# Kernel tuning notes

Measured on AMD Instinct MI355X. Metric: run time of the kernel, lower is better.

The kernel has to match this reference:

```python
import jax, jax.numpy as jnp
import numpy as np

D_MODEL = 2048
N_HEADS = 16
N_KV_HEADS = 4
D_K = D_MODEL // N_HEADS  # 128
N_REP = N_HEADS // N_KV_HEADS  # 4
EPS = 1e-8
ROPE_BASE = 10000.0


def setup_inputs() -> dict:
    key = jax.random.key(0)
    ks = jax.random.split(key, 6)
    B, S = 2, 2048
    s_in = 1.0 / np.sqrt(D_MODEL)
    return {
        "x": jax.random.normal(ks[0], (B, S, D_MODEL), jnp.float32),
        "Wq": jax.random.normal(ks[1], (D_MODEL, D_MODEL), jnp.float32) * s_in,
        "bq": jnp.zeros((D_MODEL,), jnp.float32),
        "Wk": jax.random.normal(ks[2], (N_KV_HEADS * D_K, D_MODEL), jnp.float32) * s_in,
        "bk": jnp.zeros((N_KV_HEADS * D_K,), jnp.float32),
        "Wv": jax.random.normal(ks[3], (N_KV_HEADS * D_K, D_MODEL), jnp.float32) * s_in,
        "bv": jnp.zeros((N_KV_HEADS * D_K,), jnp.float32),
        "Wo": jax.random.normal(ks[4], (D_MODEL, D_MODEL), jnp.float32) * s_in,
        "bo": jnp.zeros((D_MODEL,), jnp.float32),
        "q_norm_w": jnp.ones((D_K,), jnp.float32),
        "k_norm_w": jnp.ones((D_K,), jnp.float32),
    }


def _rmsnorm(x, w):
    rms = jnp.sqrt(jnp.mean(x * x, axis=-1, keepdims=True) + EPS)
    return x / rms * w


def _rope(x, cos, sin):
    # x: [B, S, H, d_k]; interleaved pair rotation (pairs along last dim)
    B, S, H, d = x.shape
    xr = x.reshape(B, S, H, d // 2, 2)
    x1, x2 = xr[..., 0], xr[..., 1]
    c = cos[:, None, :]  # [S, 1, d/2] -> broadcasts over [B, S, H, d/2]
    s = sin[:, None, :]
    o1 = x1 * c - x2 * s
    o2 = x1 * s + x2 * c
    return jnp.stack([o1, o2], axis=-1).reshape(B, S, H, d)


def reference(x, Wq, bq, Wk, bk, Wv, bv, Wo, bo, q_norm_w, k_norm_w):
    B, S, D = x.shape
    scale = 1.0 / np.sqrt(D_K)

    q = (x @ Wq.T + bq).reshape(B, S, N_HEADS, D_K)
    k = (x @ Wk.T + bk).reshape(B, S, N_KV_HEADS, D_K)
    v = (x @ Wv.T + bv).reshape(B, S, N_KV_HEADS, D_K)

    q = _rmsnorm(q, q_norm_w)
    k = _rmsnorm(k, k_norm_w)

    # RoPE tables (cos/sin of t * inv_freq), shape [S, d_k/2]
    inv_freq = 1.0 / (ROPE_BASE ** (jnp.arange(0, D_K, 2, dtype=jnp.float32) / D_K))
    freqs = jnp.arange(S, dtype=jnp.float32)[:, None] * inv_freq[None, :]
    cos, sin = jnp.cos(freqs), jnp.sin(freqs)
    q = _rope(q, cos, sin)
    k = _rope(k, cos, sin)

    # [B, H, S, d]
    q = q.transpose(0, 2, 1, 3)
    k = k.transpose(0, 2, 1, 3)
    v = v.transpose(0, 2, 1, 3)

    # GQA: group q heads by kv head instead of repeating k/v
    qg = q.reshape(B, N_KV_HEADS, N_REP, S, D_K)
    scores = jnp.einsum("bkrqd,bkld->bkrql", qg, k) * scale
    causal = jnp.tril(jnp.ones((S, S), dtype=bool))  # [S, S]
    scores = jnp.where(causal, scores, jnp.float32(-1e9))
    attn = jax.nn.softmax(scores, axis=-1)
    out = jnp.einsum("bkrql,bkld->bkrqd", attn, v)  # [B, Hk, rep, S, d]
    out = out.reshape(B, N_HEADS, S, D_K).transpose(0, 2, 1, 3).reshape(B, S, D)
    return out @ Wo.T + bo
```

## Files before the change

kernel.cpp:

```cpp
#include <hip/hip_runtime.h>
#include <hip/hip_bf16.h>
#include <stdint.h>

#define DM 2048
#define SQ 2048
#define NB 2
#define NH 16
#define NKV 4
#define DK 128
#define NQKV 3072

typedef unsigned short u16;
typedef unsigned int u32;
typedef __attribute__((ext_vector_type(8))) __bf16 bf16x8;
typedef __attribute__((ext_vector_type(4))) float f32x4;
typedef __attribute__((ext_vector_type(8))) u16 u16x8;
typedef __attribute__((ext_vector_type(2))) u32 u32x2;

__device__ __forceinline__ u16 f2bf(float f) {
  u32 x = __builtin_bit_cast(u32, f);
  x += 0x7fffu + ((x >> 16) & 1u);
  return (u16)(x >> 16);
}

__device__ __forceinline__ f32x4 mfma16(bf16x8 a, bf16x8 b, f32x4 c) {
  return __builtin_amdgcn_mfma_f32_16x16x32_bf16(a, b, c, 0, 0, 0);
}

#define GLDS16(g, l)                                                          \
  __builtin_amdgcn_global_load_lds(                                           \
      (const __attribute__((address_space(1))) void*)(g),                     \
      (__attribute__((address_space(3))) void*)(l), 16, 0, 0)

__global__ void cast_kernel(const float* __restrict__ src, u16* __restrict__ dst, int n8) {
  int i = blockIdx.x * blockDim.x + threadIdx.x;
  if (i >= n8) return;
  const float4* s4 = (const float4*)src;
  float4 a = s4[2 * i], b = s4[2 * i + 1];
  u16x8 v;
  v[0] = f2bf(a.x); v[1] = f2bf(a.y); v[2] = f2bf(a.z); v[3] = f2bf(a.w);
  v[4] = f2bf(b.x); v[5] = f2bf(b.y); v[6] = f2bf(b.z); v[7] = f2bf(b.w);
  *(u16x8*)(dst + 8 * (size_t)i) = v;
}

__global__ void fuse_bias(const float* __restrict__ bq, const float* __restrict__ bk,
                          const float* __restrict__ bv, float* __restrict__ fb) {
  int i = blockIdx.x * blockDim.x + threadIdx.x;
  if (i >= NQKV) return;
  float v;
  if (i < DM) v = bq[i];
  else if (i < DM + NKV * DK) v = bk[i - DM];
  else v = bv[i - DM - NKV * DK];
  fb[i] = v;
}

__global__ __launch_bounds__(256) void gemm_bt(
    const u16* __restrict__ A, const u16* __restrict__ W,
    const float* __restrict__ bias, float* __restrict__ C,
    int M, int N, int K) {
  __shared__ u16 As[128 * 64];
  __shared__ u16 Bs[128 * 64];
  const int tid = threadIdx.x;
  const int w = tid >> 6, l = tid & 63;
  const int hi = l >> 4, lo = l & 15;
  const int MB = M >> 7;
  const int nwg = gridDim.x;
  const int bid = blockIdx.x;
  const int swz = (bid & 7) * (nwg >> 3) + (bid >> 3);
  const int bm = swz % MB, bn = swz / MB;
  const int wr = w >> 1, wc = w & 1;
  const int lr8 = l >> 3, lc = l & 7;
  f32x4 acc[4][4] = {};
  for (int kt = 0; kt < K; kt += 64) {
#pragma unroll
    for (int i = 0; i < 4; ++i) {
      int row = w * 32 + i * 8 + lr8;
      int gc = lc ^ (row & 7);
      GLDS16(A + (size_t)(bm * 128 + row) * K + kt + gc * 8, &As[(w * 32 + i * 8) * 64]);
    }
#pragma unroll
    for (int i = 0; i < 4; ++i) {
      int row = w * 32 + i * 8 + lr8;
      int gc = lc ^ (row & 7);
      GLDS16(W + (size_t)(bn * 128 + row) * K + kt + gc * 8, &Bs[(w * 32 + i * 8) * 64]);
    }
    __syncthreads();
#pragma unroll
    for (int kk = 0; kk < 2; ++kk) {
      bf16x8 af[4], bf[4];
#pragma unroll
      for (int mi = 0; mi < 4; ++mi) {
        int row = wr * 64 + mi * 16 + lo;
        af[mi] = *(const bf16x8*)&As[row * 64 + (((kk * 4 + hi) ^ (row & 7)) * 8)];
      }
#pragma unroll
      for (int ni = 0; ni < 4; ++ni) {
        int row = wc * 64 + ni * 16 + lo;
        bf[ni] = *(const bf16x8*)&Bs[row * 64 + (((kk * 4 + hi) ^ (row & 7)) * 8)];
      }
#pragma unroll
      for (int mi = 0; mi < 4; ++mi)
#pragma unroll
        for (int ni = 0; ni < 4; ++ni)
          acc[mi][ni] = mfma16(af[mi], bf[ni], acc[mi][ni]);
    }
    __syncthreads();
  }
#pragma unroll
  for (int mi = 0; mi < 4; ++mi) {
#pragma unroll
    for (int ni = 0; ni < 4; ++ni) {
      int col = bn * 128 + wc * 64 + ni * 16 + lo;
      float bv = bias[col];
#pragma unroll
      for (int r = 0; r < 4; ++r) {
        int rowg = bm * 128 + wr * 64 + mi * 16 + hi * 4 + r;
        C[(size_t)rowg * N + col] = acc[mi][ni][r] + bv;
      }
    }
  }
}

__global__ void normrope_qk(const float* __restrict__ qkv,
                            const float* __restrict__ qw, const float* __restrict__ kw,
                            u16* __restrict__ qb, u16* __restrict__ kb) {
  int gw = (int)((blockIdx.x * (size_t)blockDim.x + threadIdx.x) >> 6);
  int lane = threadIdx.x & 63;
  int bs = gw / (NH + NKV), j = gw % (NH + NKV);
  int b = bs / SQ, s = bs % SQ;
  const float* src;
  const float* wgt;
  u16* dst;
  float post = 1.0f;
  if (j < NH) {
    src = qkv + (size_t)bs * NQKV + j * DK;
    wgt = qw;
    dst = qb + ((size_t)(b * NH + j) * SQ + s) * DK;
    post = 0.08838834764831845f;
  } else {
    int kh = j - NH;
    src = qkv + (size_t)bs * NQKV + DM + kh * DK;
    wgt = kw;
    dst = kb + ((size_t)(b * NKV + kh) * SQ + s) * DK;
  }
  float2 xv = *(const float2*)(src + 2 * lane);
  float ss = xv.x * xv.x + xv.y * xv.y;
#pragma unroll
  for (int m = 1; m < 64; m <<= 1) ss += __shfl_xor(ss, m);
  float inv = rsqrtf(ss * (1.0f / DK) + 1e-8f);
  float x1 = xv.x * inv * wgt[2 * lane];
  float x2 = xv.y * inv * wgt[2 * lane + 1];
  float theta = (float)s * expf((float)lane * (-9.2103403720f / 64.0f));
  float sn, cs;
  sincosf(theta, &sn, &cs);
  float o1 = (x1 * cs - x2 * sn) * post;
  float o2 = (x1 * sn + x2 * cs) * post;
  u32 pack = (u32)f2bf(o1) | ((u32)f2bf(o2) << 16);
  *(u32*)(dst + 2 * lane) = pack;
}

__global__ __launch_bounds__(256) void vtrans(const float* __restrict__ qkv, u16* __restrict__ vt) {
  __shared__ u16 T[128 * 72];
  int bid = blockIdx.x;
  int st = bid % (SQ / 64);
  int rem = bid / (SQ / 64);
  int vh = rem % NKV, b = rem / NKV;
  int s0 = st * 64;
  int t = threadIdx.x;
#pragma unroll
  for (int it = 0; it < 8; ++it) {
    int idx = it * 256 + t;
    int sl = idx >> 5;
    int c4 = idx & 31;
    float4 v = *(const float4*)(qkv + (size_t)(b * SQ + s0 + sl) * NQKV + DM + NKV * DK + vh * DK + c4 * 4);
    T[(c4 * 4 + 0) * 72 + sl] = f2bf(v.x);
    T[(c4 * 4 + 1) * 72 + sl] = f2bf(v.y);
    T[(c4 * 4 + 2) * 72 + sl] = f2bf(v.z);
    T[(c4 * 4 + 3) * 72 + sl] = f2bf(v.w);
  }
  __syncthreads();
#pragma unroll
  for (int it = 0; it < 4; ++it) {
    int idx = it * 256 + t;
    int d = idx >> 3;
    int ch = idx & 7;
    u16x8 v = *(const u16x8*)&T[d * 72 + ch * 8];
    *(u16x8*)(vt + ((size_t)(b * NKV + vh) * DK + d) * SQ + s0 + ch * 8) = v;
  }
}

__global__ __launch_bounds__(256) void attn(const u16* __restrict__ qb, const u16* __restrict__ kb,
                                            const u16* __restrict__ vt, u16* __restrict__ out) {
  __shared__ u16 Ks[2][64 * 128];
  __shared__ u16 Vs[2][128 * 64];
  __shared__ u16 P[4][16 * 64];
  const int w = threadIdx.x >> 6, l = threadIdx.x & 63;
  const int hi = l >> 4, lo = l & 15;
  const int pr = blockIdx.x, h = blockIdx.y, b = blockIdx.z;
  const int kvh = h >> 2;
  const u16* Q = qb + (size_t)(b * NH + h) * SQ * DK;
  const u16* K = kb + (size_t)(b * NKV + kvh) * SQ * DK;
  const u16* V = vt + (size_t)(b * NKV + kvh) * DK * SQ;

  auto stageKV = [&](int buf, int kt) {
#pragma unroll
    for (int i = 0; i < 4; ++i) {
      int rb = w * 16 + i * 4;
      int row = rb + (l >> 4);
      int gc = (l & 15) ^ (row & 7);
      GLDS16(K + (size_t)(kt + row) * DK + gc * 8, &Ks[buf][rb * 128]);
    }
#pragma unroll
    for (int i = 0; i < 4; ++i) {
      int rb = w * 32 + i * 8;
      int row = rb + (l >> 3);
      int gc = (l & 7) ^ (row & 7);
      GLDS16(V + (size_t)row * SQ + kt + gc * 8, &Vs[buf][rb * 64]);
    }
  };

#pragma unroll 1
  for (int seg = 0; seg < 2; ++seg) {
    const int qt = seg ? (SQ / 64 - 1 - pr) : pr;
    const int q0 = qt * 64 + w * 16;
    bf16x8 qf[4];
#pragma unroll
    for (int kk = 0; kk < 4; ++kk)
      qf[kk] = *(const bf16x8*)(Q + (size_t)(q0 + lo) * DK + kk * 32 + hi * 8);
    f32x4 oacc[8] = {};
    float lrun = 0.f;
    const int nt = qt + 1;
    stageKV(0, 0);
    __syncthreads();
#pragma unroll 1
    for (int ti = 0; ti < nt; ++ti) {
      const int cur = ti & 1;
      if (ti + 1 < nt) stageKV(cur ^ 1, (ti + 1) * 64);
      const int kt = ti * 64;
      f32x4 sfr[4];
      __builtin_amdgcn_s_setprio(1);
#pragma unroll
      for (int cb = 0; cb < 4; ++cb) {
        f32x4 sf = {};
#pragma unroll
        for (int kk = 0; kk < 4; ++kk) {
          int row = cb * 16 + lo;
          bf16x8 kfr = *(const bf16x8*)&Ks[cur][row * 128 + (((kk * 4 + hi) ^ (row & 7)) * 8)];
          sf = mfma16(kfr, qf[kk], sf);
        }
        sfr[cb] = sf;
      }
      __builtin_amdgcn_s_setprio(0);
      if (ti == nt - 1) {
#pragma unroll
        for (int cb = 0; cb < 4; ++cb)
#pragma unroll
          for (int r = 0; r < 4; ++r) {
            int kcol = kt + cb * 16 + hi * 4 + r;
            if (kcol > q0 + lo) sfr[cb][r] = -1e9f;
          }
      }
      float rs = 0.f;
#pragma unroll
      for (int cb = 0; cb < 4; ++cb) {
        float p0 = __expf(sfr[cb][0] - 12.0f);
        float p1 = __expf(sfr[cb][1] - 12.0f);
        float p2 = __expf(sfr[cb][2] - 12.0f);
        float p3 = __expf(sfr[cb][3] - 12.0f);
        rs += (p0 + p1) + (p2 + p3);
        u32x2 pw;
        pw[0] = (u32)f2bf(p0) | ((u32)f2bf(p1) << 16);
        pw[1] = (u32)f2bf(p2) | ((u32)f2bf(p3) << 16);
        int chunk = cb * 2 + (hi >> 1);
        *(u32x2*)&P[w][lo * 64 + ((chunk ^ (lo & 7)) * 8) + (hi & 1) * 4] = pw;
      }
      rs += __shfl_xor(rs, 16);
      rs += __shfl_xor(rs, 32);
      lrun += rs;
      __builtin_amdgcn_s_setprio(1);
#pragma unroll
      for (int half = 0; half < 2; ++half) {
        bf16x8 pa = *(const bf16x8*)&P[w][lo * 64 + (((half * 4 + hi) ^ (lo & 7)) * 8)];
#pragma unroll
        for (int fr = 0; fr < 8; ++fr) {
          int row = fr * 16 + lo;
          bf16x8 vfr = *(const bf16x8*)&Vs[cur][row * 64 + (((half * 4 + hi) ^ (row & 7)) * 8)];
          oacc[fr] = mfma16(pa, vfr, oacc[fr]);
        }
      }
      __builtin_amdgcn_s_setprio(0);
      __syncthreads();
    }
    float invl = 1.0f / lrun;
    float invlB[4];
#pragma unroll
    for (int r = 0; r < 4; ++r) invlB[r] = __shfl(invl, hi * 4 + r);
#pragma unroll
    for (int fr = 0; fr < 8; ++fr) {
#pragma unroll
      for (int r = 0; r < 4; ++r) {
        int row = b * SQ + q0 + hi * 4 + r;
        int col = h * DK + fr * 16 + lo;
        out[(size_t)row * DM + col] = f2bf(oacc[fr][r] * invlB[r]);
      }
    }
  }
}

extern "C" void kernel_launch(void* const* d_in, const int* in_sizes, int n_in,
                              void* d_out, int out_size, void* d_ws, size_t ws_size,
                              hipStream_t stream) {
  const float* x = (const float*)d_in[0];
  const float* Wq = (const float*)d_in[1];
  const float* bq = (const float*)d_in[2];
  const float* Wk = (const float*)d_in[3];
  const float* bk = (const float*)d_in[4];
  const float* Wv = (const float*)d_in[5];
  const float* bv = (const float*)d_in[6];
  const float* Wo = (const float*)d_in[7];
  const float* bo = (const float*)d_in[8];
  const float* qw = (const float*)d_in[9];
  const float* kw = (const float*)d_in[10];
  float* outp = (float*)d_out;

  char* ws = (char*)d_ws;
  size_t off = 0;
  auto alloc = [&](size_t bytes) {
    char* p = ws + off;
    off += (bytes + 255) & ~(size_t)255;
    return p;
  };
  u16* xb = (u16*)alloc((size_t)NB * SQ * DM * 2);
  u16* Wqkvb = (u16*)alloc((size_t)NQKV * DM * 2);
  u16* Wob = (u16*)alloc((size_t)DM * DM * 2);
  float* fbias = (float*)alloc((size_t)NQKV * 4);
  float* qkvf = (float*)alloc((size_t)NB * SQ * NQKV * 4);
  u16* qbh = (u16*)alloc((size_t)NB * NH * SQ * DK * 2);
  u16* kbh = (u16*)alloc((size_t)NB * NKV * SQ * DK * 2);
  u16* vth = (u16*)alloc((size_t)NB * NKV * DK * SQ * 2);
  u16* aout = (u16*)alloc((size_t)NB * SQ * DM * 2);

  {
    int n8 = NB * SQ * DM / 8;
    cast_kernel<<<(n8 + 255) / 256, 256, 0, stream>>>(x, xb, n8);
    n8 = DM * DM / 8;
    cast_kernel<<<(n8 + 255) / 256, 256, 0, stream>>>(Wq, Wqkvb, n8);
    cast_kernel<<<(n8 + 255) / 256, 256, 0, stream>>>(Wo, Wob, n8);
    n8 = NKV * DK * DM / 8;
    cast_kernel<<<(n8 + 255) / 256, 256, 0, stream>>>(Wk, Wqkvb + (size_t)DM * DM, n8);
    cast_kernel<<<(n8 + 255) / 256, 256, 0, stream>>>(Wv, Wqkvb + (size_t)(DM + NKV * DK) * DM, n8);
    fuse_bias<<<(NQKV + 255) / 256, 256, 0, stream>>>(bq, bk, bv, fbias);
  }
  {
    int M = NB * SQ;
    gemm_bt<<<(M / 128) * (NQKV / 128), 256, 0, stream>>>(xb, Wqkvb, fbias, qkvf, M, NQKV, DM);
  }
  {
    int waves = NB * SQ * (NH + NKV);
    normrope_qk<<<waves / 4, 256, 0, stream>>>(qkvf, qw, kw, qbh, kbh);
    vtrans<<<NB * NKV * (SQ / 64), 256, 0, stream>>>(qkvf, vth);
  }
  {
    dim3 g(SQ / 128, NH, NB);
    attn<<<g, 256, 0, stream>>>(qbh, kbh, vth, aout);
  }
  {
    int M = NB * SQ;
    gemm_bt<<<(M / 128) * (DM / 128), 256, 0, stream>>>(aout, Wob, bo, outp, M, DM, DM);
  }
}
```

Measured before the change: 235.8 us.

## Fuse setup casts, store QKV intermediate in bf16, precompute RoPE tables

```diff
diff --git a/kernel.cpp b/kernel.cpp
--- a/kernel.cpp
+++ b/kernel.cpp
@@ -23,6 +23,11 @@
   return (u16)(x >> 16);
 }
 
+__device__ __forceinline__ float bf2f(u16 h) {
+  u32 x = ((u32)h) << 16;
+  return __builtin_bit_cast(float, x);
+}
+
 __device__ __forceinline__ f32x4 mfma16(bf16x8 a, bf16x8 b, f32x4 c) {
   return __builtin_amdgcn_mfma_f32_16x16x32_bf16(a, b, c, 0, 0, 0);
 }
@@ -32,42 +37,60 @@
       (const __attribute__((address_space(1))) void*)(g),                     \
       (__attribute__((address_space(3))) void*)(l), 16, 0, 0)
 
-__global__ void cast_kernel(const float* __restrict__ src, u16* __restrict__ dst, int n8) {
+#define N_CAST 2359296
+#define N_ROPE (SQ * 64)
+__global__ void setup_all(const float* __restrict__ x, const float* __restrict__ Wq,
+                          const float* __restrict__ Wk, const float* __restrict__ Wv,
+                          const float* __restrict__ Wo, const float* __restrict__ bq,
+                          const float* __restrict__ bk, const float* __restrict__ bv,
+                          u16* __restrict__ xb, u16* __restrict__ Wqkvb, u16* __restrict__ Wob,
+                          float* __restrict__ ct, float* __restrict__ st_,
+                          float* __restrict__ fb) {
   int i = blockIdx.x * blockDim.x + threadIdx.x;
-  if (i >= n8) return;
-  const float4* s4 = (const float4*)src;
-  float4 a = s4[2 * i], b = s4[2 * i + 1];
-  u16x8 v;
-  v[0] = f2bf(a.x); v[1] = f2bf(a.y); v[2] = f2bf(a.z); v[3] = f2bf(a.w);
-  v[4] = f2bf(b.x); v[5] = f2bf(b.y); v[6] = f2bf(b.z); v[7] = f2bf(b.w);
-  *(u16x8*)(dst + 8 * (size_t)i) = v;
-}
-
-__global__ void fuse_bias(const float* __restrict__ bq, const float* __restrict__ bk,
-                          const float* __restrict__ bv, float* __restrict__ fb) {
-  int i = blockIdx.x * blockDim.x + threadIdx.x;
-  if (i >= NQKV) return;
-  float v;
-  if (i < DM) v = bq[i];
-  else if (i < DM + NKV * DK) v = bk[i - DM];
-  else v = bv[i - DM - NKV * DK];
-  fb[i] = v;
+  if (i < N_CAST) {
+    const float* src;
+    u16* dst;
+    int j;
+    if (i < 1048576) { src = x; dst = xb; j = i; }
+    else if (i < 1572864) { src = Wq; dst = Wqkvb; j = i - 1048576; }
+    else if (i < 1703936) { src = Wk; dst = Wqkvb + (size_t)DM * DM; j = i - 1572864; }
+    else if (i < 1835008) { src = Wv; dst = Wqkvb + (size_t)(DM + NKV * DK) * DM; j = i - 1703936; }
+    else { src = Wo; dst = Wob; j = i - 1835008; }
+    const float4* s4 = (const float4*)src;
+    float4 a = s4[2 * j], b = s4[2 * j + 1];
+    u16x8 v;
+    v[0] = f2bf(a.x); v[1] = f2bf(a.y); v[2] = f2bf(a.z); v[3] = f2bf(a.w);
+    v[4] = f2bf(b.x); v[5] = f2bf(b.y); v[6] = f2bf(b.z); v[7] = f2bf(b.w);
+    *(u16x8*)(dst + 8 * (size_t)j) = v;
+  } else if (i < N_CAST + N_ROPE) {
+    int j = i - N_CAST;
+    int s = j >> 6, d = j & 63;
+    float theta = (float)s * __expf((float)d * (-9.2103403720f / 64.0f));
+    float sn, cs;
+    sincosf(theta, &sn, &cs);
+    ct[j] = cs;
+    st_[j] = sn;
+  } else if (i < N_CAST + N_ROPE + NQKV) {
+    int j = i - N_CAST - N_ROPE;
+    float v;
+    if (j < DM) v = bq[j];
+    else if (j < DM + NKV * DK) v = bk[j - DM];
+    else v = bv[j - DM - NKV * DK];
+    fb[j] = v;
+  }
 }
 
 __global__ __launch_bounds__(256) void gemm_bt(
     const u16* __restrict__ A, const u16* __restrict__ W,
-    const float* __restrict__ bias, float* __restrict__ C,
-    int M, int N, int K) {
+    const float* __restrict__ bias, void* __restrict__ Cv,
+    int M, int N, int K, int obf16) {
   __shared__ u16 As[128 * 64];
   __shared__ u16 Bs[128 * 64];
   const int tid = threadIdx.x;
   const int w = tid >> 6, l = tid & 63;
   const int hi = l >> 4, lo = l & 15;
   const int MB = M >> 7;
-  const int nwg = gridDim.x;
-  const int bid = blockIdx.x;
-  const int swz = (bid & 7) * (nwg >> 3) + (bid >> 3);
-  const int bm = swz % MB, bn = swz / MB;
+  const int bm = blockIdx.x % MB, bn = blockIdx.x / MB;
   const int wr = w >> 1, wc = w & 1;
   const int lr8 = l >> 3, lc = l & 7;
   f32x4 acc[4][4] = {};
@@ -115,20 +138,25 @@
 #pragma unroll
       for (int r = 0; r < 4; ++r) {
         int rowg = bm * 128 + wr * 64 + mi * 16 + hi * 4 + r;
-        C[(size_t)rowg * N + col] = acc[mi][ni][r] + bv;
-      }
-    }
-  }
-}
-
-__global__ void normrope_qk(const float* __restrict__ qkv,
+        float val = acc[mi][ni][r] + bv;
+        if (obf16)
+          ((u16*)Cv)[(size_t)rowg * N + col] = f2bf(val);
+        else
+          ((float*)Cv)[(size_t)rowg * N + col] = val;
+      }
+    }
+  }
+}
+
+__global__ void normrope_qk(const u16* __restrict__ qkv,
                             const float* __restrict__ qw, const float* __restrict__ kw,
+                            const float* __restrict__ cosT, const float* __restrict__ sinT,
                             u16* __restrict__ qb, u16* __restrict__ kb) {
   int gw = (int)((blockIdx.x * (size_t)blockDim.x + threadIdx.x) >> 6);
   int lane = threadIdx.x & 63;
   int bs = gw / (NH + NKV), j = gw % (NH + NKV);
   int b = bs / SQ, s = bs % SQ;
-  const float* src;
+  const u16* src;
   const float* wgt;
   u16* dst;
   float post = 1.0f;
@@ -143,23 +171,24 @@
     wgt = kw;
     dst = kb + ((size_t)(b * NKV + kh) * SQ + s) * DK;
   }
-  float2 xv = *(const float2*)(src + 2 * lane);
-  float ss = xv.x * xv.x + xv.y * xv.y;
+  u32 pk = *(const u32*)(src + 2 * lane);
+  float xv0 = bf2f((u16)(pk & 0xffff));
+  float xv1 = bf2f((u16)(pk >> 16));
+  float ss = xv0 * xv0 + xv1 * xv1;
 #pragma unroll
   for (int m = 1; m < 64; m <<= 1) ss += __shfl_xor(ss, m);
   float inv = rsqrtf(ss * (1.0f / DK) + 1e-8f);
-  float x1 = xv.x * inv * wgt[2 * lane];
-  float x2 = xv.y * inv * wgt[2 * lane + 1];
-  float theta = (float)s * expf((float)lane * (-9.2103403720f / 64.0f));
-  float sn, cs;
-  sincosf(theta, &sn, &cs);
+  float x1 = xv0 * inv * wgt[2 * lane];
+  float x2 = xv1 * inv * wgt[2 * lane + 1];
+  float cs = cosT[s * 64 + lane];
+  float sn = sinT[s * 64 + lane];
   float o1 = (x1 * cs - x2 * sn) * post;
   float o2 = (x1 * sn + x2 * cs) * post;
   u32 pack = (u32)f2bf(o1) | ((u32)f2bf(o2) << 16);
   *(u32*)(dst + 2 * lane) = pack;
 }
 
-__global__ __launch_bounds__(256) void vtrans(const float* __restrict__ qkv, u16* __restrict__ vt) {
+__global__ __launch_bounds__(256) void vtrans(const u16* __restrict__ qkv, u16* __restrict__ vt) {
   __shared__ u16 T[128 * 72];
   int bid = blockIdx.x;
   int st = bid % (SQ / 64);
@@ -168,15 +197,13 @@
   int s0 = st * 64;
   int t = threadIdx.x;
 #pragma unroll
-  for (int it = 0; it < 8; ++it) {
+  for (int it = 0; it < 4; ++it) {
     int idx = it * 256 + t;
-    int sl = idx >> 5;
-    int c4 = idx & 31;
-    float4 v = *(const float4*)(qkv + (size_t)(b * SQ + s0 + sl) * NQKV + DM + NKV * DK + vh * DK + c4 * 4);
-    T[(c4 * 4 + 0) * 72 + sl] = f2bf(v.x);
-    T[(c4 * 4 + 1) * 72 + sl] = f2bf(v.y);
-    T[(c4 * 4 + 2) * 72 + sl] = f2bf(v.z);
-    T[(c4 * 4 + 3) * 72 + sl] = f2bf(v.w);
+    int sl = idx >> 4;
+    int c = idx & 15;
+    u16x8 v = *(const u16x8*)(qkv + (size_t)(b * SQ + s0 + sl) * NQKV + DM + NKV * DK + vh * DK + c * 8);
+#pragma unroll
+    for (int e = 0; e < 8; ++e) T[(c * 8 + e) * 72 + sl] = v[e];
   }
   __syncthreads();
 #pragma unroll
@@ -334,31 +361,27 @@
   u16* Wqkvb = (u16*)alloc((size_t)NQKV * DM * 2);
   u16* Wob = (u16*)alloc((size_t)DM * DM * 2);
   float* fbias = (float*)alloc((size_t)NQKV * 4);
-  float* qkvf = (float*)alloc((size_t)NB * SQ * NQKV * 4);
+  float* cosT = (float*)alloc((size_t)SQ * 64 * 4);
+  float* sinT = (float*)alloc((size_t)SQ * 64 * 4);
+  u16* qkvb = (u16*)alloc((size_t)NB * SQ * NQKV * 2);
   u16* qbh = (u16*)alloc((size_t)NB * NH * SQ * DK * 2);
   u16* kbh = (u16*)alloc((size_t)NB * NKV * SQ * DK * 2);
   u16* vth = (u16*)alloc((size_t)NB * NKV * DK * SQ * 2);
   u16* aout = (u16*)alloc((size_t)NB * SQ * DM * 2);
 
   {
-    int n8 = NB * SQ * DM / 8;
-    cast_kernel<<<(n8 + 255) / 256, 256, 0, stream>>>(x, xb, n8);
-    n8 = DM * DM / 8;
-    cast_kernel<<<(n8 + 255) / 256, 256, 0, stream>>>(Wq, Wqkvb, n8);
-    cast_kernel<<<(n8 + 255) / 256, 256, 0, stream>>>(Wo, Wob, n8);
-    n8 = NKV * DK * DM / 8;
-    cast_kernel<<<(n8 + 255) / 256, 256, 0, stream>>>(Wk, Wqkvb + (size_t)DM * DM, n8);
-    cast_kernel<<<(n8 + 255) / 256, 256, 0, stream>>>(Wv, Wqkvb + (size_t)(DM + NKV * DK) * DM, n8);
-    fuse_bias<<<(NQKV + 255) / 256, 256, 0, stream>>>(bq, bk, bv, fbias);
+    int total = N_CAST + N_ROPE + NQKV;
+    setup_all<<<(total + 255) / 256, 256, 0, stream>>>(x, Wq, Wk, Wv, Wo, bq, bk, bv,
+                                                       xb, Wqkvb, Wob, cosT, sinT, fbias);
   }
   {
     int M = NB * SQ;
-    gemm_bt<<<(M / 128) * (NQKV / 128), 256, 0, stream>>>(xb, Wqkvb, fbias, qkvf, M, NQKV, DM);
+    gemm_bt<<<(M / 128) * (NQKV / 128), 256, 0, stream>>>(xb, Wqkvb, fbias, qkvb, M, NQKV, DM, 1);
   }
   {
     int waves = NB * SQ * (NH + NKV);
-    normrope_qk<<<waves / 4, 256, 0, stream>>>(qkvf, qw, kw, qbh, kbh);
-    vtrans<<<NB * NKV * (SQ / 64), 256, 0, stream>>>(qkvf, vth);
+    normrope_qk<<<waves / 4, 256, 0, stream>>>(qkvb, qw, kw, cosT, sinT, qbh, kbh);
+    vtrans<<<NB * NKV * (SQ / 64), 256, 0, stream>>>(qkvb, vth);
   }
   {
     dim3 g(SQ / 128, NH, NB);
@@ -366,6 +389,6 @@
   }
   {
     int M = NB * SQ;
-    gemm_bt<<<(M / 128) * (DM / 128), 256, 0, stream>>>(aout, Wob, bo, outp, M, DM, DM);
-  }
-}
+    gemm_bt<<<(M / 128) * (DM / 128), 256, 0, stream>>>(aout, Wob, bo, outp, M, DM, DM, 0);
+  }
+}
```

Result: faster. 216.8 us, median of 3 (-8.0%).
